# Kernel optimization log

Measured on AMD Instinct MI355X. Metric: run time of the kernel, lower is better.

## Reference

```python
import jax, jax.numpy as jnp
import numpy as np

H, W = 4096, 4096
KH, KW = 11, 11


def setup_inputs() -> dict:
    key = jax.random.key(0)
    k1, k2 = jax.random.split(key)
    x = jax.random.normal(k1, (H, W), dtype=jnp.float32)
    weight = jax.random.uniform(k2, (KH, KW), dtype=jnp.float32)
    bias = jnp.zeros((1,), dtype=jnp.float32)
    return {"x": x, "weight": weight, "bias": bias}


def reference(x, weight, bias):
    # corr2d: valid 2D cross-correlation of a single-channel image with a
    # single kernel, then add scalar bias. Output shape [H-KH+1, W-KW+1].
    out = jax.lax.conv_general_dilated(
        x[None, None, :, :],            # NCHW, N=C=1
        weight[None, None, :, :],       # OIHW, O=I=1
        window_strides=(1, 1),
        padding="VALID",
        dimension_numbers=("NCHW", "OIHW", "NCHW"),
    )[0, 0]
    return out + bias[0]
```

## Files before the change

### kernel.cpp

```cpp
#include <hip/hip_runtime.h>
#include <hip/hip_bf16.h>

#define IH 4096
#define IW 4096
#define KH 11
#define KW 11
#define OH (IH - KH + 1)
#define OW (IW - KW + 1)

#define BM 64
#define BN 64
#define TROWS   74
#define TSTRIDE 84
#define NC4     20
#define NCHUNK  (TROWS * NC4)
#define NITER   6
#define TILE_SHORTS (TROWS * TSTRIDE)

#define TILES_X 64
#define NPAIR   2048
#define BMAT_SHORTS (KH * 512)

typedef short bf16x4 __attribute__((ext_vector_type(4)));
typedef short bf16x8 __attribute__((ext_vector_type(8)));
typedef float f32x4  __attribute__((ext_vector_type(4)));

__device__ __forceinline__ short f2b(float f) {
    __hip_bfloat16 h = __float2bfloat16(f);
    return __builtin_bit_cast(short, h);
}

__global__ void build_bmat(const float* __restrict__ w, short* __restrict__ bm) {
    const int tid = threadIdx.x;
#pragma unroll
    for (int t = 0; t < 22; ++t) {
        const int idx = tid + t * 256;
        const int kh = idx >> 9;
        const int j  = (idx >> 5) & 15;
        const int k  = idx & 31;
        const int d  = k - j;
        const float val = (d >= 0 && d < KW) ? w[kh * KW + d] : 0.f;
        bm[idx] = f2b(val);
    }
}

__device__ __forceinline__ void stage_load(float4 G[NITER],
                                           const float* __restrict__ x,
                                           int gx0, int gy0, int tid) {
#pragma unroll
    for (int it = 0; it < NITER; ++it) {
        const int i = tid + it * 256;
        float4 v = make_float4(0.f, 0.f, 0.f, 0.f);
        if (i < NCHUNK) {
            const int r  = i / NC4;
            const int c4 = i - r * NC4;
            const int gy = gy0 + r;
            const int gx = gx0 + c4 * 4;
            if (gy < IH && gx + 3 < IW) {
                v = *reinterpret_cast<const float4*>(x + (size_t)gy * IW + gx);
            }
        }
        G[it] = v;
    }
}

__device__ __forceinline__ void stage_write(short* __restrict__ tb,
                                            const float4 G[NITER], int tid) {
#pragma unroll
    for (int it = 0; it < NITER; ++it) {
        const int i = tid + it * 256;
        if (i < NCHUNK) {
            const int r  = i / NC4;
            const int c4 = i - r * NC4;
            bf16x4 b = { f2b(G[it].x), f2b(G[it].y), f2b(G[it].z), f2b(G[it].w) };
            *reinterpret_cast<bf16x4*>(&tb[r * TSTRIDE + c4 * 4]) = b;
        }
    }
}

__device__ __forceinline__ void loadA(bf16x8 a[4], const short* __restrict__ ap) {
#pragma unroll
    for (int c = 0; c < 4; ++c) {
        bf16x4 lo = *reinterpret_cast<const bf16x4*>(ap + c * 16);
        bf16x4 hi = *reinterpret_cast<const bf16x4*>(ap + c * 16 + 4);
        a[c] = __builtin_shufflevector(lo, hi, 0, 1, 2, 3, 4, 5, 6, 7);
    }
}

__device__ __forceinline__ void mfma4(f32x4 acc[4], const bf16x8 a[4], bf16x8 b) {
#pragma unroll
    for (int c = 0; c < 4; ++c) {
        acc[c] = __builtin_amdgcn_mfma_f32_16x16x32_bf16(a[c], b, acc[c], 0, 0, 0);
    }
}

__device__ __forceinline__ void compute_tile(const short* __restrict__ tb,
                                             const short* __restrict__ bg,
                                             float bv, float* __restrict__ out,
                                             int gx0, int gy0,
                                             int wv, int g, int li) {
    f32x4 acc[4] = {};
    const short* ap = &tb[(16 * wv + li) * TSTRIDE + g * 8];
    const short* bp = &bg[li * 32 + g * 8];

    bf16x8 Ae[4], Ao[4], Be, Bo;
    loadA(Ae, ap);
    Be = *reinterpret_cast<const bf16x8*>(bp);

#pragma unroll 1
    for (int kh2 = 0; kh2 < 5; ++kh2) {
        loadA(Ao, ap + TSTRIDE);
        Bo = *reinterpret_cast<const bf16x8*>(bp + 512);
        mfma4(acc, Ae, Be);
        ap += 2 * TSTRIDE;
        bp += 1024;
        loadA(Ae, ap);
        Be = *reinterpret_cast<const bf16x8*>(bp);
        mfma4(acc, Ao, Bo);
    }
    mfma4(acc, Ae, Be);

#pragma unroll
    for (int c = 0; c < 4; ++c) {
        const int ox = gx0 + c * 16 + li;
        if (ox < OW) {
#pragma unroll
            for (int r = 0; r < 4; ++r) {
                const int oy = gy0 + wv * 16 + g * 4 + r;
                if (oy < OH) {
                    out[(size_t)oy * OW + ox] = acc[c][r] + bv;
                }
            }
        }
    }
}

__global__ __launch_bounds__(256)
void conv2d_g(const float* __restrict__ x,
              const short* __restrict__ bg,
              const float* __restrict__ bias,
              float* __restrict__ out) {
    __shared__ short buf[2][TILE_SHORTS];

    const int tid = threadIdx.x;
    const int pair = (blockIdx.x & 7) * (NPAIR / 8) + (blockIdx.x >> 3);
    const int t0   = pair * 2;
    const int gy0  = (t0 >> 6) * BM;
    const int gxb  = (t0 & (TILES_X - 1)) * BN;

    const int lane = tid & 63;
    const int wv   = tid >> 6;
    const int g    = lane >> 4;
    const int li   = lane & 15;
    const float bv = bias[0];

    {
        float4 G0[NITER];
        stage_load(G0, x, gxb, gy0, tid);
        stage_write(buf[0], G0, tid);
    }
    __syncthreads();

    float4 G[NITER];
    stage_load(G, x, gxb + BN, gy0, tid);
    __builtin_amdgcn_sched_barrier(0);

    compute_tile(buf[0], bg, bv, out, gxb, gy0, wv, g, li);

    stage_write(buf[1], G, tid);
    __syncthreads();

    compute_tile(buf[1], bg, bv, out, gxb + BN, gy0, wv, g, li);
}

extern "C" void kernel_launch(void* const* d_in, const int* in_sizes, int n_in,
                              void* d_out, int out_size, void* d_ws, size_t ws_size,
                              hipStream_t stream) {
    const float* x    = (const float*)d_in[0];
    const float* w    = (const float*)d_in[1];
    const float* bias = (const float*)d_in[2];
    float* out        = (float*)d_out;
    short* bm         = (short*)d_ws;

    build_bmat<<<dim3(1), dim3(256), 0, stream>>>(w, bm);

    dim3 grid(NPAIR);
    dim3 block(256);
    conv2d_g<<<grid, block, 0, stream>>>(x, bm, bias, out);
}
```

Baseline: 43.88 us.

## Use one tile per block and stage the weight matrix in LDS

```diff
diff --git a/kernel.cpp b/kernel.cpp
--- a/kernel.cpp
+++ b/kernel.cpp
@@ -16,10 +16,10 @@
 #define NCHUNK  (TROWS * NC4)
 #define NITER   6
 #define TILE_SHORTS (TROWS * TSTRIDE)
+#define BMAT_SHORTS (KH * 512)
 
 #define TILES_X 64
-#define NPAIR   2048
-#define BMAT_SHORTS (KH * 512)
+#define NTILE   4096
 
 typedef short bf16x4 __attribute__((ext_vector_type(4)));
 typedef short bf16x8 __attribute__((ext_vector_type(8)));
@@ -44,40 +44,6 @@
     }
 }
 
-__device__ __forceinline__ void stage_load(float4 G[NITER],
-                                           const float* __restrict__ x,
-                                           int gx0, int gy0, int tid) {
-#pragma unroll
-    for (int it = 0; it < NITER; ++it) {
-        const int i = tid + it * 256;
-        float4 v = make_float4(0.f, 0.f, 0.f, 0.f);
-        if (i < NCHUNK) {
-            const int r  = i / NC4;
-            const int c4 = i - r * NC4;
-            const int gy = gy0 + r;
-            const int gx = gx0 + c4 * 4;
-            if (gy < IH && gx + 3 < IW) {
-                v = *reinterpret_cast<const float4*>(x + (size_t)gy * IW + gx);
-            }
-        }
-        G[it] = v;
-    }
-}
-
-__device__ __forceinline__ void stage_write(short* __restrict__ tb,
-                                            const float4 G[NITER], int tid) {
-#pragma unroll
-    for (int it = 0; it < NITER; ++it) {
-        const int i = tid + it * 256;
-        if (i < NCHUNK) {
-            const int r  = i / NC4;
-            const int c4 = i - r * NC4;
-            bf16x4 b = { f2b(G[it].x), f2b(G[it].y), f2b(G[it].z), f2b(G[it].w) };
-            *reinterpret_cast<bf16x4*>(&tb[r * TSTRIDE + c4 * 4]) = b;
-        }
-    }
-}
-
 __device__ __forceinline__ void loadA(bf16x8 a[4], const short* __restrict__ ap) {
 #pragma unroll
     for (int c = 0; c < 4; ++c) {
@@ -94,14 +60,53 @@
     }
 }
 
-__device__ __forceinline__ void compute_tile(const short* __restrict__ tb,
-                                             const short* __restrict__ bg,
-                                             float bv, float* __restrict__ out,
-                                             int gx0, int gy0,
-                                             int wv, int g, int li) {
+__global__ __launch_bounds__(256)
+void conv2d_tlp(const float* __restrict__ x,
+                const short* __restrict__ bg,
+                const float* __restrict__ bias,
+                float* __restrict__ out) {
+    __shared__ short lds[TILE_SHORTS + BMAT_SHORTS];
+
+    const int tid = threadIdx.x;
+    const int blk = (blockIdx.x & 7) * (NTILE / 8) + (blockIdx.x >> 3);
+    const int gy0 = (blk >> 6) * BM;
+    const int gx0 = (blk & (TILES_X - 1)) * BN;
+
+    const int lane = tid & 63;
+    const int wv   = tid >> 6;
+    const int g    = lane >> 4;
+    const int li   = lane & 15;
+    const float bv = bias[0];
+
+#pragma unroll
+    for (int it = 0; it < NITER; ++it) {
+        const int i = tid + it * 256;
+        if (i < NCHUNK) {
+            const int r  = i / NC4;
+            const int c4 = i - r * NC4;
+            const int gy = gy0 + r;
+            const int gx = gx0 + c4 * 4;
+            float4 v = make_float4(0.f, 0.f, 0.f, 0.f);
+            if (gy < IH && gx + 3 < IW) {
+                v = *reinterpret_cast<const float4*>(x + (size_t)gy * IW + gx);
+            }
+            bf16x4 b = { f2b(v.x), f2b(v.y), f2b(v.z), f2b(v.w) };
+            *reinterpret_cast<bf16x4*>(&lds[r * TSTRIDE + c4 * 4]) = b;
+        }
+    }
+#pragma unroll
+    for (int t = 0; t < 3; ++t) {
+        const int idx = tid + t * 256;
+        if (idx < (BMAT_SHORTS * 2) / 16) {
+            reinterpret_cast<int4*>(&lds[TILE_SHORTS])[idx] =
+                reinterpret_cast<const int4*>(bg)[idx];
+        }
+    }
+    __syncthreads();
+
     f32x4 acc[4] = {};
-    const short* ap = &tb[(16 * wv + li) * TSTRIDE + g * 8];
-    const short* bp = &bg[li * 32 + g * 8];
+    const short* ap = &lds[(16 * wv + li) * TSTRIDE + g * 8];
+    const short* bp = &lds[TILE_SHORTS + li * 32 + g * 8];
 
     bf16x8 Ae[4], Ao[4], Be, Bo;
     loadA(Ae, ap);
@@ -135,44 +140,6 @@
     }
 }
 
-__global__ __launch_bounds__(256)
-void conv2d_g(const float* __restrict__ x,
-              const short* __restrict__ bg,
-              const float* __restrict__ bias,
-              float* __restrict__ out) {
-    __shared__ short buf[2][TILE_SHORTS];
-
-    const int tid = threadIdx.x;
-    const int pair = (blockIdx.x & 7) * (NPAIR / 8) + (blockIdx.x >> 3);
-    const int t0   = pair * 2;
-    const int gy0  = (t0 >> 6) * BM;
-    const int gxb  = (t0 & (TILES_X - 1)) * BN;
-
-    const int lane = tid & 63;
-    const int wv   = tid >> 6;
-    const int g    = lane >> 4;
-    const int li   = lane & 15;
-    const float bv = bias[0];
-
-    {
-        float4 G0[NITER];
-        stage_load(G0, x, gxb, gy0, tid);
-        stage_write(buf[0], G0, tid);
-    }
-    __syncthreads();
-
-    float4 G[NITER];
-    stage_load(G, x, gxb + BN, gy0, tid);
-    __builtin_amdgcn_sched_barrier(0);
-
-    compute_tile(buf[0], bg, bv, out, gxb, gy0, wv, g, li);
-
-    stage_write(buf[1], G, tid);
-    __syncthreads();
-
-    compute_tile(buf[1], bg, bv, out, gxb + BN, gy0, wv, g, li);
-}
-
 extern "C" void kernel_launch(void* const* d_in, const int* in_sizes, int n_in,
                               void* d_out, int out_size, void* d_ws, size_t ws_size,
                               hipStream_t stream) {
@@ -184,7 +151,7 @@
 
     build_bmat<<<dim3(1), dim3(256), 0, stream>>>(w, bm);
 
-    dim3 grid(NPAIR);
+    dim3 grid(NTILE);
     dim3 block(256);
-    conv2d_g<<<grid, block, 0, stream>>>(x, bm, bias, out);
+    conv2d_tlp<<<grid, block, 0, stream>>>(x, bm, bias, out);
 }
```

New measurement: 38.79 us. 1.13x faster.

## Use 8 waves per block splitting tile columns and stage weight matrix in LDS

Applied to the files above, without the earlier changes.

```diff
diff --git a/kernel.cpp b/kernel.cpp
--- a/kernel.cpp
+++ b/kernel.cpp
@@ -14,12 +14,12 @@
 #define TSTRIDE 84
 #define NC4     20
 #define NCHUNK  (TROWS * NC4)
-#define NITER   6
+#define NITER   3
 #define TILE_SHORTS (TROWS * TSTRIDE)
+#define BMAT_SHORTS (KH * 512)
 
 #define TILES_X 64
 #define NPAIR   2048
-#define BMAT_SHORTS (KH * 512)
 
 typedef short bf16x4 __attribute__((ext_vector_type(4)));
 typedef short bf16x8 __attribute__((ext_vector_type(8)));
@@ -49,7 +49,7 @@
                                            int gx0, int gy0, int tid) {
 #pragma unroll
     for (int it = 0; it < NITER; ++it) {
-        const int i = tid + it * 256;
+        const int i = tid + it * 512;
         float4 v = make_float4(0.f, 0.f, 0.f, 0.f);
         if (i < NCHUNK) {
             const int r  = i / NC4;
@@ -68,7 +68,7 @@
                                             const float4 G[NITER], int tid) {
 #pragma unroll
     for (int it = 0; it < NITER; ++it) {
-        const int i = tid + it * 256;
+        const int i = tid + it * 512;
         if (i < NCHUNK) {
             const int r  = i / NC4;
             const int c4 = i - r * NC4;
@@ -78,55 +78,55 @@
     }
 }
 
-__device__ __forceinline__ void loadA(bf16x8 a[4], const short* __restrict__ ap) {
-#pragma unroll
-    for (int c = 0; c < 4; ++c) {
+__device__ __forceinline__ void loadA2(bf16x8 a[2], const short* __restrict__ ap) {
+#pragma unroll
+    for (int c = 0; c < 2; ++c) {
         bf16x4 lo = *reinterpret_cast<const bf16x4*>(ap + c * 16);
         bf16x4 hi = *reinterpret_cast<const bf16x4*>(ap + c * 16 + 4);
         a[c] = __builtin_shufflevector(lo, hi, 0, 1, 2, 3, 4, 5, 6, 7);
     }
 }
 
-__device__ __forceinline__ void mfma4(f32x4 acc[4], const bf16x8 a[4], bf16x8 b) {
-#pragma unroll
-    for (int c = 0; c < 4; ++c) {
+__device__ __forceinline__ void mfma2(f32x4 acc[2], const bf16x8 a[2], bf16x8 b) {
+#pragma unroll
+    for (int c = 0; c < 2; ++c) {
         acc[c] = __builtin_amdgcn_mfma_f32_16x16x32_bf16(a[c], b, acc[c], 0, 0, 0);
     }
 }
 
 __device__ __forceinline__ void compute_tile(const short* __restrict__ tb,
-                                             const short* __restrict__ bg,
+                                             const short* __restrict__ bmat,
                                              float bv, float* __restrict__ out,
                                              int gx0, int gy0,
-                                             int wv, int g, int li) {
-    f32x4 acc[4] = {};
-    const short* ap = &tb[(16 * wv + li) * TSTRIDE + g * 8];
-    const short* bp = &bg[li * 32 + g * 8];
-
-    bf16x8 Ae[4], Ao[4], Be, Bo;
-    loadA(Ae, ap);
+                                             int wr, int ch, int g, int li) {
+    f32x4 acc[2] = {};
+    const short* ap = &tb[(16 * wr + li) * TSTRIDE + ch * 32 + g * 8];
+    const short* bp = &bmat[li * 32 + g * 8];
+
+    bf16x8 Ae[2], Ao[2], Be, Bo;
+    loadA2(Ae, ap);
     Be = *reinterpret_cast<const bf16x8*>(bp);
 
 #pragma unroll 1
     for (int kh2 = 0; kh2 < 5; ++kh2) {
-        loadA(Ao, ap + TSTRIDE);
+        loadA2(Ao, ap + TSTRIDE);
         Bo = *reinterpret_cast<const bf16x8*>(bp + 512);
-        mfma4(acc, Ae, Be);
+        mfma2(acc, Ae, Be);
         ap += 2 * TSTRIDE;
         bp += 1024;
-        loadA(Ae, ap);
+        loadA2(Ae, ap);
         Be = *reinterpret_cast<const bf16x8*>(bp);
-        mfma4(acc, Ao, Bo);
-    }
-    mfma4(acc, Ae, Be);
-
-#pragma unroll
-    for (int c = 0; c < 4; ++c) {
-        const int ox = gx0 + c * 16 + li;
+        mfma2(acc, Ao, Bo);
+    }
+    mfma2(acc, Ae, Be);
+
+#pragma unroll
+    for (int c = 0; c < 2; ++c) {
+        const int ox = gx0 + ch * 32 + c * 16 + li;
         if (ox < OW) {
 #pragma unroll
             for (int r = 0; r < 4; ++r) {
-                const int oy = gy0 + wv * 16 + g * 4 + r;
+                const int oy = gy0 + wr * 16 + g * 4 + r;
                 if (oy < OH) {
                     out[(size_t)oy * OW + ox] = acc[c][r] + bv;
                 }
@@ -135,12 +135,13 @@
     }
 }
 
-__global__ __launch_bounds__(256)
-void conv2d_g(const float* __restrict__ x,
-              const short* __restrict__ bg,
-              const float* __restrict__ bias,
-              float* __restrict__ out) {
+__global__ __launch_bounds__(512)
+void conv2d_w8(const float* __restrict__ x,
+               const short* __restrict__ bg,
+               const float* __restrict__ bias,
+               float* __restrict__ out) {
     __shared__ short buf[2][TILE_SHORTS];
+    __shared__ short bmat[BMAT_SHORTS];
 
     const int tid = threadIdx.x;
     const int pair = (blockIdx.x & 7) * (NPAIR / 8) + (blockIdx.x >> 3);
@@ -150,6 +151,8 @@
 
     const int lane = tid & 63;
     const int wv   = tid >> 6;
+    const int wr   = wv >> 1;
+    const int ch   = wv & 1;
     const int g    = lane >> 4;
     const int li   = lane & 15;
     const float bv = bias[0];
@@ -159,18 +162,26 @@
         stage_load(G0, x, gxb, gy0, tid);
         stage_write(buf[0], G0, tid);
     }
+#pragma unroll
+    for (int t = 0; t < 2; ++t) {
+        const int idx = tid + t * 512;
+        if (idx < (BMAT_SHORTS * 2) / 16) {
+            reinterpret_cast<int4*>(bmat)[idx] =
+                reinterpret_cast<const int4*>(bg)[idx];
+        }
+    }
     __syncthreads();
 
     float4 G[NITER];
     stage_load(G, x, gxb + BN, gy0, tid);
     __builtin_amdgcn_sched_barrier(0);
 
-    compute_tile(buf[0], bg, bv, out, gxb, gy0, wv, g, li);
+    compute_tile(buf[0], bmat, bv, out, gxb, gy0, wr, ch, g, li);
 
     stage_write(buf[1], G, tid);
     __syncthreads();
 
-    compute_tile(buf[1], bg, bv, out, gxb + BN, gy0, wv, g, li);
+    compute_tile(buf[1], bmat, bv, out, gxb + BN, gy0, wr, ch, g, li);
 }
 
 extern "C" void kernel_launch(void* const* d_in, const int* in_sizes, int n_in,
@@ -185,6 +196,6 @@
     build_bmat<<<dim3(1), dim3(256), 0, stream>>>(w, bm);
 
     dim3 grid(NPAIR);
-    dim3 block(256);
-    conv2d_g<<<grid, block, 0, stream>>>(x, bm, bias, out);
-}
+    dim3 block(512);
+    conv2d_w8<<<grid, block, 0, stream>>>(x, bm, bias, out);
+}
```

Result: faster. 40.58 us (-7.5%).
